# Kernel optimization log

Hardware: AMD Instinct MI355X
Metric: run time of the kernel (lower is better)

Reference implementation:

```python
import jax, jax.numpy as jnp
import numpy as np

SR = 44100
DUR = 2.0
DS = 64
IN_GAIN = 10.0 ** (5.2 / 20.0)


def design_lr4_ir(freq, sr, n_taps=512):
    wc = np.tan(np.pi * freq / sr)
    wc2 = wc * wc
    root2 = np.sqrt(2.0)
    denom = 1 + root2 * wc + wc2
    b_lp = np.array([wc2 / denom, 2 * wc2 / denom, wc2 / denom])
    a_lp = np.array([1.0, 2 * (wc2 - 1) / denom, (1 - root2 * wc + wc2) / denom])
    b_hp = np.array([1 / denom, -2 / denom, 1 / denom])
    a_hp = np.array([1.0, 2 * (wc2 - 1) / denom, (1 - root2 * wc + wc2) / denom])
    b_lp4 = np.convolve(b_lp, b_lp); a_lp4 = np.convolve(a_lp, a_lp)
    b_hp4 = np.convolve(b_hp, b_hp); a_hp4 = np.convolve(a_hp, a_hp)
    def lfilter(b, a, x):
        y = np.zeros_like(x)
        for n in range(len(x)):
            acc = 0.0
            for i in range(len(b)):
                if n - i >= 0:
                    acc += b[i] * x[n - i]
            for i in range(1, len(a)):
                if n - i >= 0:
                    acc -= a[i] * y[n - i]
            y[n] = acc
        return y
    imp = np.zeros(n_taps); imp[0] = 1.0
    return lfilter(b_lp4, a_lp4, imp), lfilter(b_hp4, a_hp4, imp)


def _fir(x, w):
    # x: [B,C,T], w: flipped IR [K]; causal (left) padding, same filter per channel (grouped)
    K = w.shape[0]; C = x.shape[1]
    xp = jnp.pad(x, ((0, 0), (0, 0), (K - 1, 0)))
    kern = jnp.broadcast_to(w.reshape(1, 1, K), (C, 1, K))
    return jax.lax.conv_general_dilated(xp, kern, (1,), 'VALID',
                                        dimension_numbers=('NCH', 'OIH', 'NCH'),
                                        feature_group_count=C)


def _conv1d(x, w, b, pad, dil):
    y = jax.lax.conv_general_dilated(x, w, (1,), [(pad, pad)], rhs_dilation=(dil,),
                                     dimension_numbers=('NCH', 'OIH', 'NCH'))
    return y + b[None, :, None]


def _knee(x, thr, slope, k):
    diff = x - thr
    g_knee = slope * (diff + k / 2) ** 2 / (2 * k)
    return jnp.where(jnp.abs(diff) <= k / 2, g_knee,
                     jnp.where(diff > k / 2, slope * diff, jnp.zeros_like(x)))


def _forward(audio, params, rel_alphas, knee_db, ir_low_lp, ir_low_hp, ir_high_lp, ir_high_hp,
             w0, b0, w1, b1, w2, b2, w3, b3, w4, b4):
    batch, C, T = audio.shape
    audio_in = audio * IN_GAIN
    ott = params[:, -7:]
    amount = ott[:, 0][:, None, None]
    # 3-band LR4 crossover via 512-tap FIRs
    low = _fir(audio_in, ir_low_lp)
    m_h = _fir(audio_in, ir_low_hp)
    mid = _fir(m_h, ir_high_lp)
    high = _fir(m_h, ir_high_hp)
    bands = jnp.stack([high, mid, low], axis=1)            # [B,3,2,T]
    b_flat = bands.reshape(batch * 3, C, T)
    x_sq = jnp.mean(b_flat ** 2, axis=1, keepdims=True)    # [B3,1,T]
    Tc = T // DS
    x_rms = jnp.sqrt(x_sq[..., :Tc * DS].reshape(batch * 3, 1, Tc, DS).mean(-1) + 1e-7)
    # release-only envelope follower via cummax trick (faithful to torch code incl. repeat order)
    rel = jnp.repeat(rel_alphas, batch).reshape(-1, 1, 1)
    k = 1.0 - rel
    idx = jnp.arange(Tc, dtype=x_rms.dtype)
    kp = k ** idx
    ki = k ** (-idx)
    env_c = jax.lax.cummax(x_rms * ki, axis=2) * kp        # [B3,1,Tc]
    # linear interp back to T (align_corners=True)
    pos = jnp.arange(T, dtype=jnp.float32) * ((Tc - 1) / (T - 1))
    i0 = jnp.clip(jnp.floor(pos).astype(jnp.int32), 0, Tc - 2)
    frac = pos - i0.astype(jnp.float32)
    env = jnp.take(env_c, i0, axis=2) * (1 - frac) + jnp.take(env_c, i0 + 1, axis=2) * frac
    env_db = 20.0 * jnp.log10(env + 1e-7).reshape(batch, 3, T)
    t_a = jnp.stack([ott[:, 3], ott[:, 2], ott[:, 1]], axis=1)[..., None]
    t_b = jnp.stack([ott[:, 6], ott[:, 5], ott[:, 4]], axis=1)[..., None]
    above_slopes = jnp.array([1.0, 1.0 - 1 / 66.7, 1.0 - 1 / 66.7], jnp.float32).reshape(1, 3, 1)
    below_slope = jnp.float32(1.0 - 1.0 / 4.17)
    g_db = -_knee(env_db, t_a, above_slopes, knee_db) + _knee(-env_db, -t_b, below_slope, knee_db)
    out_gains = jnp.array([10.3, 5.7, 10.3], jnp.float32).reshape(1, 3, 1)
    total_g = 10.0 ** (jnp.clip(g_db + out_gains, -80.0, 40.0) / 20.0)
    combined = (bands * total_g[:, :, None, :]).sum(axis=1)  # [B,2,T]
    g = lambda z: jax.nn.gelu(z, approximate=False)
    r = g(_conv1d(combined, w0, b0, 1, 1))
    r = g(_conv1d(r, w1, b1, 2, 2))
    r = g(_conv1d(r, w2, b2, 4, 4))
    r = g(_conv1d(r, w3, b3, 8, 8))
    res = _conv1d(r, w4, b4, 1, 1)
    return (1.0 - amount) * audio + amount * (combined + res)


def setup_inputs() -> dict:
    B = 8
    T = int(SR * DUR)
    key = jax.random.key(0)
    ks = jax.random.split(key, 16)
    audio = jax.random.normal(ks[0], (B, 2, T), jnp.float32)
    amount = jax.random.uniform(ks[1], (B, 1), jnp.float32)
    thr = jax.random.uniform(ks[2], (B, 6), jnp.float32, minval=-40.0, maxval=0.0)
    params = jnp.concatenate([amount, thr], axis=1)
    ir_lp1, ir_hp1 = design_lr4_ir(88.3, SR)
    ir_lp2, ir_hp2 = design_lr4_ir(2500.0, SR)
    flip = lambda ir: jnp.asarray(ir[::-1].copy(), jnp.float32)
    sr_c = SR / DS
    rel_alphas = jnp.asarray(1.0 - np.exp(-1.0 / (sr_c * np.array([132.0, 282.0, 282.0]) / 1000.0)), jnp.float32)
    knee_db = jnp.float32(3.0)
    shapes = [(64, 2, 3), (64, 64, 3), (64, 64, 3), (64, 64, 3), (2, 64, 3)]
    out = {
        'audio': audio, 'params': params, 'rel_alphas': rel_alphas, 'knee_db': knee_db,
        'ir_low_lp': flip(ir_lp1), 'ir_low_hp': flip(ir_hp1),
        'ir_high_lp': flip(ir_lp2), 'ir_high_hp': flip(ir_hp2),
    }
    for i, (o, ci, kk) in enumerate(shapes):
        bound = 1.0 / np.sqrt(ci * kk)
        scale = 0.01 if i == len(shapes) - 1 else 1.0
        out[f'w{i}'] = jax.random.uniform(ks[4 + 2 * i], (o, ci, kk), jnp.float32, -bound, bound) * scale
        out[f'b{i}'] = jax.random.uniform(ks[5 + 2 * i], (o,), jnp.float32, -bound, bound) * scale
    return out


def reference(audio, params, rel_alphas, knee_db, ir_low_lp, ir_low_hp, ir_high_lp, ir_high_hp,
              w0, b0, w1, b1, w2, b2, w3, b3, w4, b4):
    return _forward(audio, params, rel_alphas, knee_db, ir_low_lp, ir_low_hp, ir_high_lp, ir_high_hp,
                    w0, b0, w1, b1, w2, b2, w3, b3, w4, b4)
```

## Files before the change

### kernel.cpp

```cpp
#include <hip/hip_runtime.h>
#include <math.h>

#define NT 88200
#define NB 8
#define TC 1378

static constexpr float IN_GAIN_F = 1.8197008586099834f;

#define OFF_A0    3072
#define OFF_A4    4096
#define OFF_ABF   5632
#define OFF_BANDS 24064
#define OFF_XRMS  4257664
#define OFF_ENV   4290736
#define OFF_WHL   4290736

typedef __attribute__((ext_vector_type(8))) short short8v;
typedef __attribute__((ext_vector_type(4))) short short4v;
typedef __attribute__((ext_vector_type(4))) float float4v;
typedef __attribute__((ext_vector_type(16))) float float16v;

__device__ __forceinline__ float gelus(float x) {
  float e = __builtin_amdgcn_exp2f(-2.4554670f * x);
  return x * __builtin_amdgcn_rcpf(1.f + e);
}
__device__ __forceinline__ short f2bf(float x) {
  unsigned int u = __float_as_uint(x);
  u += 0x7fffu + ((u >> 16) & 1u);
  return (short)(u >> 16);
}
__device__ __forceinline__ short f2bft(float x) {
  return (short)(__float_as_uint(x) >> 16);
}
__device__ __forceinline__ float bf2f(short s) {
  return __uint_as_float(((unsigned int)(unsigned short)s) << 16);
}

__global__ __launch_bounds__(256) void k_prep(
    const float* __restrict__ irLL, const float* __restrict__ irLH,
    const float* __restrict__ irHL, const float* __restrict__ irHH,
    const float* __restrict__ w0, const float* __restrict__ w1,
    const float* __restrict__ w2, const float* __restrict__ w3,
    const float* __restrict__ w4, float* __restrict__ ws)
{
  int gid = blockIdx.x * 256 + threadIdx.x;
  int task = blockIdx.y;
  if (task == 0) {
    short* whl = (short*)(ws + OFF_WHL);
    if (gid < 3072) {
      int band = gid >> 10, j = gid & 1023;
      float v = 0.f;
      if (j < 1023) {
        if (band == 2) {
          v = (j >= 511) ? irLL[j - 511] : 0.f;
        } else {
          const float* wb = (band == 0) ? irHH : irHL;
          int lo = j - 511; if (lo < 0) lo = 0;
          int hi = (j < 511) ? j : 511;
          float acc = 0.f;
          for (int i = lo; i <= hi; ++i) acc += irLH[i] * wb[j - i];
          v = acc;
        }
      }
      int entry = band * 1152 + 64 + j;
      short h = f2bf(v);
      whl[entry] = h;
      whl[entry + 4608] = f2bf(v - bf2f(h));
    } else if (gid < 4608) {
      int z = gid - 3072;
      int entry;
      if (z < 384) {
        int band = z >> 7, r = z & 127;
        entry = band * 1152 + (r < 64 ? r : 1024 + r);
      } else {
        entry = 3 * 1152 + (z - 384);
      }
      whl[entry] = 0;
      whl[entry + 4608] = 0;
    }
  } else if (task == 1) {
    if (gid >= 2048) return;
    int wq = gid >> 9;
    int lane = (gid >> 3) & 63;
    int j = gid & 7;
    int l16 = lane & 15, q = lane >> 4;
    int m = wq * 16 + l16;
    int K = q * 8 + j;
    float val = (K < 6) ? w0[(m * 2 + (K & 1)) * 3 + (K >> 1)] : 0.f;
    ((short*)(ws + OFF_A0))[gid] = f2bf(val);
  } else if (task == 2) {
    if (gid >= 3072) return;
    int s = gid >> 9;
    int lane = (gid - s * 512) >> 3;
    int j = gid & 7;
    int m = lane & 15, q = lane >> 4;
    int K = s * 32 + q * 8 + j;
    int k = K >> 6, ic = K & 63;
    float val = (m < 2) ? w4[(m * 64 + ic) * 3 + k] : 0.f;
    ((short*)(ws + OFF_A4))[gid] = f2bf(val);
  } else if (task == 6) {
    for (int r = 0; r < 3; ++r) {
      int i = gid * 3 + r;
      if (i < 24 * TC) ws[OFF_XRMS + i] = 0.f;
    }
  } else {
    int l = task - 3;
    if (gid >= 12288) return;
    const float* wl = (l == 0) ? w1 : (l == 1) ? w2 : w3;
    int ocg = gid / 6144;
    int rem = gid - ocg * 6144;
    int s = rem / 512;
    int rem2 = rem - s * 512;
    int lane = rem2 >> 3;
    int j = gid & 7;
    int m = ocg * 32 + (lane & 31);
    int k = s * 16 + ((lane >> 5) << 3) + j;
    int tap = k >> 6, ic = k & 63;
    short* ap = (short*)(ws + OFF_ABF);
    ap[l * 12288 + gid] = f2bf(wl[(m * 64 + ic) * 3 + tap]);
  }
}

#define FT 320
__global__ __launch_bounds__(256) void k_firm(const float* __restrict__ audio,
                                              float* __restrict__ ws)
{
  __shared__ short xh[4][1360];
  __shared__ __align__(16) short wt[9216];
  __shared__ float ssum[3][5];
  int bc = blockIdx.x, tile = blockIdx.y;
  int t0b = tile * FT;
  int tid = threadIdx.x;
  if (tid < 15) ssum[tid / 5][tid % 5] = 0.f;
  const uint4* wsrc = (const uint4*)((const short*)(ws + OFF_WHL));
  uint4* wdst = (uint4*)wt;
  for (int i = tid; i < 1152; i += 256) wdst[i] = wsrc[i];
  const float* x = audio + bc * NT;
  for (int i = tid; i < 1363; i += 256) {
    int g = t0b - 1022 + i;
    float v = (g >= 0 && g < NT) ? x[g] * IN_GAIN_F : 0.f;
    short h = f2bf(v);
#pragma unroll
    for (int c = 0; c < 4; ++c) {
      int idx = i - c;
      if (idx >= 0 && idx < 1360) xh[c][idx] = h;
    }
  }
  __syncthreads();

  int wave = tid >> 6, lane = tid & 63;
  int q = lane >> 4, l16 = lane & 15;
  int band = (l16 >= 10) ? 2 : (l16 >= 5 ? 1 : 0);
  if (l16 == 15) band = 3;
  int u = l16 - band * 5;
  const short* pAh = wt + band * 1152 + 64 + q * 8 - u * 16;
  const short* pAl = pAh + 4608;
  int c = l16 & 3;
  int xoff = wave * 80 + q * 8 + ((l16 >> 2) << 2);
  const short* pBh = &xh[c][xoff];
  float4v a0 = {0.f, 0.f, 0.f, 0.f};
  float4v a1 = {0.f, 0.f, 0.f, 0.f};
#pragma unroll 2
  for (int s = 0; s < 34; ++s) {
    short8v ah = *(const short8v*)(pAh + 32 * s);
    short8v al = *(const short8v*)(pAl + 32 * s);
    short4v bh0 = *(const short4v*)(pBh + 32 * s);
    short4v bh1 = *(const short4v*)(pBh + 32 * s + 4);
    short8v bh = __builtin_shufflevector(bh0, bh1, 0, 1, 2, 3, 4, 5, 6, 7);
    a0 = __builtin_amdgcn_mfma_f32_16x16x32_bf16(ah, bh, a0, 0, 0, 0);
    a1 = __builtin_amdgcn_mfma_f32_16x16x32_bf16(al, bh, a1, 0, 0, 0);
  }
  float acc[4];
#pragma unroll
  for (int r = 0; r < 4; ++r) acc[r] = a0[r] + a1[r];

  int b = bc >> 1, ch = bc & 1;
  float* bands = ws + OFF_BANDS;
#pragma unroll
  for (int r = 0; r < 4; ++r) {
    int m = q * 4 + r;
    if (m < 15) {
      int bnd = (m >= 10) ? 2 : (m >= 5 ? 1 : 0);
      int uu = m - bnd * 5;
      int t = t0b + wave * 80 + uu * 16 + l16;
      if (t < NT) bands[((b * 3 + bnd) * 2 + ch) * NT + t] = acc[r];
    }
  }

  float s2[4];
#pragma unroll
  for (int r = 0; r < 4; ++r) {
    int m = q * 4 + r;
    s2[r] = (m < 15) ? acc[r] * acc[r] : 0.f;
  }
#pragma unroll
  for (int mask = 1; mask < 16; mask <<= 1)
#pragma unroll
    for (int r = 0; r < 4; ++r)
      s2[r] += __shfl_xor(s2[r], mask, 16);
  if (l16 == 0) {
#pragma unroll
    for (int r = 0; r < 4; ++r) {
      int m = q * 4 + r;
      if (m < 15) {
        int bnd = (m >= 10) ? 2 : (m >= 5 ? 1 : 0);
        int uu = m - bnd * 5;
        int jloc = (wave * 80 + uu * 16) >> 6;
        atomicAdd(&ssum[bnd][jloc], s2[r]);
      }
    }
  }
  __syncthreads();
  if (tid < 15) {
    int bnd = tid / 5, jl = tid - bnd * 5;
    int jg = tile * 5 + jl;
    if (jg < TC) atomicAdd(&ws[OFF_XRMS + (b * 3 + bnd) * TC + jg], ssum[bnd][jl]);
  }
}

__global__ __launch_bounds__(256) void k_scan(const float* __restrict__ rel_alphas,
                                              float* __restrict__ ws)
{
  __shared__ float pA[256], pB[256];
  int row = blockIdx.x;
  int tid = threadIdx.x;
  float kdec = 1.f - rel_alphas[row >> 3];
  const float* xr = ws + OFF_XRMS + row * TC;
  float v[6];
  int base = tid * 6;
#pragma unroll
  for (int s = 0; s < 6; ++s) {
    int j = base + s;
    v[s] = (j < TC) ? sqrtf(xr[j] * (0.5f / 64.f) + 1e-7f) : 0.f;
  }
  float r = v[0];
#pragma unroll
  for (int s = 1; s < 6; ++s) r = fmaxf(v[s], r * kdec);
  pA[tid] = r;
  __syncthreads();
  float k2 = kdec * kdec, k3 = k2 * kdec;
  float kp = k3 * k3;
  float* in = pA; float* outp = pB;
  for (int off = 1; off < 256; off <<= 1) {
    float val = in[tid];
    if (tid >= off) val = fmaxf(val, in[tid - off] * kp);
    outp[tid] = val;
    kp *= kp;
    __syncthreads();
    float* tmp = in; in = outp; outp = tmp;
  }
  float* env = ws + OFF_ENV + row * TC;
  float rr;
  if (tid > 0) {
    float carry = in[tid - 1];
    rr = fmaxf(v[0], carry * kdec);
  } else {
    rr = v[0];
  }
  if (base < TC) env[base] = rr;
#pragma unroll
  for (int s = 1; s < 6; ++s) {
    rr = fmaxf(v[s], rr * kdec);
    if (base + s < TC) env[base + s] = rr;
  }
}

#define PITCH 72
#define SPAN 128
#define TILE 96

__device__ __forceinline__ void mfma_layer32(const short* in, short* outb,
    const short* __restrict__ apk, const float* __restrict__ bias,
    const int d, int t0, int ocg, int posg, int lane)
{
  int l32 = lane & 31, hi = lane >> 5;
  float16v acc;
#pragma unroll
  for (int g = 0; g < 4; ++g) {
    float4 bv = *(const float4*)&bias[ocg * 32 + hi * 4 + g * 8];
    acc[4 * g + 0] = bv.x; acc[4 * g + 1] = bv.y;
    acc[4 * g + 2] = bv.z; acc[4 * g + 3] = bv.w;
  }
  int rbase = posg * 32 + l32;
  int rlo = rbase - d; rlo = rlo < 0 ? 0 : rlo;
  int rhi = rbase + d; rhi = rhi > SPAN - 1 ? SPAN - 1 : rhi;
  const short* pLo  = in + rlo * PITCH + hi * 8;
  const short* pMid = in + rbase * PITCH + hi * 8;
  const short* pHi  = in + rhi * PITCH + hi * 8;
  const short* ap = apk + (ocg * 12 * 64 + lane) * 8;
#pragma unroll
  for (int s = 0; s < 12; ++s) {
    short8v a = *(const short8v*)(ap + s * 512);
    int tap = s >> 2;
    const short* p = (tap == 0) ? pLo : (tap == 1) ? pMid : pHi;
    short8v bf = *(const short8v*)(p + (s & 3) * 16);
    acc = __builtin_amdgcn_mfma_f32_32x32x16_bf16(a, bf, acc, 0, 0, 0);
  }
  int t = t0 - 16 + rbase;
  bool z = (t < 0) | (t >= NT);
  short* wp = outb + rbase * PITCH + ocg * 32 + hi * 4;
#pragma unroll
  for (int g = 0; g < 4; ++g) {
    short4v r;
#pragma unroll
    for (int q = 0; q < 4; ++q)
      r[q] = f2bft(z ? 0.f : gelus(acc[4 * g + q]));
    *(short4v*)(wp + g * 8) = r;
  }
}

__global__ __launch_bounds__(512, 8) void k_convnet(
    const float* __restrict__ audio, const float* __restrict__ params,
    const float* __restrict__ kneep,
    const float* __restrict__ b0, const float* __restrict__ b1,
    const float* __restrict__ b2, const float* __restrict__ b3,
    const float* __restrict__ b4, const float* __restrict__ ws,
    float* __restrict__ out)
{
  __shared__ float cmb[2][SPAN];
  __shared__ __align__(16) char ubuf[SPAN * 8 * 2];
  __shared__ __align__(16) short actA[SPAN * PITCH];
  __shared__ __align__(16) short actB[SPAN * PITCH];
  float* gbuf = (float*)ubuf;
  short (*bfL0)[8] = (short(*)[8])ubuf;
  int tile = blockIdx.x, b = blockIdx.y;
  int t0 = tile * TILE;
  int tid = threadIdx.x;
  int wave = tid >> 6, lane = tid & 63;

  if (tid < 3 * SPAN) {
    int band = tid / SPAN, pos = tid - band * SPAN;
    int t = t0 - 16 + pos;
    float g = 0.f;
    if (t >= 0 && t < NT) {
      const float* env = ws + OFF_ENV;
      float knee = kneep[0];
      float halfk = 0.5f * knee;
      float inv2k = 1.f / (2.f * knee);
      const float scale = (float)(1377.0 / 88199.0);
      float pos_f = (float)t * scale;
      int i0 = (int)floorf(pos_f);
      i0 = i0 < 0 ? 0 : (i0 > TC - 2 ? TC - 2 : i0);
      float frac = pos_f - (float)i0;
      const int tacol[3] = {3, 2, 1};
      const int tbcol[3] = {6, 5, 4};
      const float asl[3] = {1.f, (float)(1.0 - 1.0 / 66.7), (float)(1.0 - 1.0 / 66.7)};
      const float bsl = (float)(1.0 - 1.0 / 4.17);
      const float og[3] = {10.3f, 5.7f, 10.3f};
      int row = b * 3 + band;
      float e = env[row * TC + i0] * (1.f - frac) + env[row * TC + i0 + 1] * frac;
      float edb = 6.0205999132796239f * __builtin_amdgcn_logf(e + 1e-7f);
      float ta = params[b * 7 + tacol[band]];
      float tb = params[b * 7 + tbcol[band]];
      float d1 = edb - ta;
      float gk1 = asl[band] * (d1 + halfk) * (d1 + halfk) * inv2k;
      float ka = (fabsf(d1) <= halfk) ? gk1 : (d1 > halfk ? asl[band] * d1 : 0.f);
      float d2 = tb - edb;
      float gk2 = bsl * (d2 + halfk) * (d2 + halfk) * inv2k;
      float kb = (fabsf(d2) <= halfk) ? gk2 : (d2 > halfk ? bsl * d2 : 0.f);
      float gdb = -ka + kb + og[band];
      gdb = fminf(fmaxf(gdb, -80.f), 40.f);
      g = __builtin_amdgcn_exp2f(gdb * 0.16609640474436812f);
    }
    gbuf[band * SPAN + pos] = g;
  }
  __syncthreads();

  if (tid < SPAN) {
    int t = t0 - 16 + tid;
    float c0 = 0.f, c1 = 0.f;
    if (t >= 0 && t < NT) {
      const float* bands = ws + OFF_BANDS;
#pragma unroll
      for (int band = 0; band < 3; ++band) {
        int row = b * 3 + band;
        float g = gbuf[band * SPAN + tid];
        c0 += bands[(row * 2 + 0) * NT + t] * g;
        c1 += bands[(row * 2 + 1) * NT + t] * g;
      }
    }
    cmb[0][tid] = c0;
    cmb[1][tid] = c1;
  }
  __syncthreads();

  for (int i = tid; i < SPAN * 8; i += 512) {
    int r = i >> 3, j = i & 7;
    short v = 0;
    if (j < 6) {
      int k = j >> 1, ic = j & 1;
      int src = r - 1 + k;
      if (src >= 0 && src < SPAN) v = f2bf(cmb[ic][src]);
    }
    bfL0[r][j] = v;
  }
  __syncthreads();

  int quad = lane >> 4, l16 = lane & 15;

  {
    int wq = wave & 3, half = wave >> 2;
    const short* ap0 = (const short*)(ws + OFF_A0);
    short8v a0 = *(const short8v*)&ap0[(wq * 64 + lane) * 8];
    float4 bv = *(const float4*)&b0[wq * 16 + quad * 4];
    float4v acc[4];
#pragma unroll
    for (int n = 0; n < 4; ++n) { acc[n][0] = bv.x; acc[n][1] = bv.y; acc[n][2] = bv.z; acc[n][3] = bv.w; }
    short8v zf = {0, 0, 0, 0, 0, 0, 0, 0};
#pragma unroll
    for (int n = 0; n < 4; ++n) {
      int row = (half * 4 + n) * 16 + l16;
      short8v bf = (quad == 0) ? *(const short8v*)&bfL0[row][0] : zf;
      acc[n] = __builtin_amdgcn_mfma_f32_16x16x32_bf16(a0, bf, acc[n], 0, 0, 0);
    }
    int ocb = wq * 16 + quad * 4;
#pragma unroll
    for (int n = 0; n < 4; ++n) {
      int p = (half * 4 + n) * 16 + l16;
      int t = t0 - 16 + p;
      bool z = (t < 0) | (t >= NT);
      short4v r;
#pragma unroll
      for (int rg = 0; rg < 4; ++rg)
        r[rg] = f2bft(z ? 0.f : gelus(acc[n][rg]));
      *(short4v*)&actA[p * PITCH + ocb] = r;
    }
  }
  __syncthreads();

  int ocg = wave & 1, posg = wave >> 1;
  const short* apk = (const short*)(ws + OFF_ABF);
  mfma_layer32(actA, actB, apk,          b1, 2, t0, ocg, posg, lane);
  __syncthreads();
  mfma_layer32(actB, actA, apk + 12288,  b2, 4, t0, ocg, posg, lane);
  __syncthreads();
  mfma_layer32(actA, actB, apk + 24576,  b3, 8, t0, ocg, posg, lane);
  __syncthreads();

  if (wave < 6) {
    const short* ap4 = (const short*)(ws + OFF_A4);
    float4v acc = {0.f, 0.f, 0.f, 0.f};
    if (quad == 0) { acc[0] = b4[0]; acc[1] = b4[1]; }
#pragma unroll
    for (int s = 0; s < 6; ++s) {
      short8v a4 = *(const short8v*)&ap4[(s * 64 + lane) * 8];
      int kt = s >> 1;
      int ic0 = (s & 1) * 32 + quad * 8;
      int row = 16 + wave * 16 + l16 + kt - 1;
      short8v bf = *(const short8v*)&actB[row * PITCH + ic0];
      acc = __builtin_amdgcn_mfma_f32_16x16x32_bf16(a4, bf, acc, 0, 0, 0);
    }
    if (quad == 0) {
      int t = t0 + wave * 16 + l16;
      if (t < NT) {
        float amt = params[b * 7];
#pragma unroll
        for (int r = 0; r < 2; ++r) {
          float aud = audio[(b * 2 + r) * NT + t];
          out[(b * 2 + r) * NT + t] =
              (1.f - amt) * aud + amt * (cmb[r][16 + wave * 16 + l16] + acc[r]);
        }
      }
    }
  }
}

extern "C" void kernel_launch(void* const* d_in, const int* in_sizes, int n_in,
                              void* d_out, int out_size, void* d_ws, size_t ws_size,
                              hipStream_t stream)
{
  (void)in_sizes; (void)n_in; (void)out_size; (void)ws_size;
  const float* audio = (const float*)d_in[0];
  const float* params = (const float*)d_in[1];
  const float* rel   = (const float*)d_in[2];
  const float* knee  = (const float*)d_in[3];
  const float* irLL  = (const float*)d_in[4];
  const float* irLH  = (const float*)d_in[5];
  const float* irHL  = (const float*)d_in[6];
  const float* irHH  = (const float*)d_in[7];
  const float* w0 = (const float*)d_in[8];  const float* b0 = (const float*)d_in[9];
  const float* w1 = (const float*)d_in[10]; const float* b1 = (const float*)d_in[11];
  const float* w2 = (const float*)d_in[12]; const float* b2 = (const float*)d_in[13];
  const float* w3 = (const float*)d_in[14]; const float* b3 = (const float*)d_in[15];
  const float* w4 = (const float*)d_in[16]; const float* b4 = (const float*)d_in[17];
  float* out = (float*)d_out;
  float* ws  = (float*)d_ws;

  hipLaunchKernelGGL(k_prep, dim3(48, 7), dim3(256), 0, stream,
                     irLL, irLH, irHL, irHH, w0, w1, w2, w3, w4, ws);
  hipLaunchKernelGGL(k_firm, dim3(16, 276), dim3(256), 0, stream, audio, ws);
  hipLaunchKernelGGL(k_scan, dim3(24), dim3(256), 0, stream, rel, ws);
  hipLaunchKernelGGL(k_convnet, dim3(919, 8), dim3(512), 0, stream,
                     audio, params, knee, b0, b1, b2, b3, b4, ws, out);
}
```

Measured before the change: 295.5 us.

## Enlarge convnet tile to 256 positions and pack bf16 conversions

Result: slower. 301.6 us (+2.1%).

```diff
diff --git a/kernel.cpp b/kernel.cpp
--- a/kernel.cpp
+++ b/kernel.cpp
@@ -17,6 +17,7 @@
 
 typedef __attribute__((ext_vector_type(8))) short short8v;
 typedef __attribute__((ext_vector_type(4))) short short4v;
+typedef __attribute__((ext_vector_type(2))) unsigned int uint2v;
 typedef __attribute__((ext_vector_type(4))) float float4v;
 typedef __attribute__((ext_vector_type(16))) float float16v;
 
@@ -29,11 +30,13 @@
   u += 0x7fffu + ((u >> 16) & 1u);
   return (short)(u >> 16);
 }
-__device__ __forceinline__ short f2bft(float x) {
-  return (short)(__float_as_uint(x) >> 16);
-}
 __device__ __forceinline__ float bf2f(short s) {
   return __uint_as_float(((unsigned int)(unsigned short)s) << 16);
+}
+__device__ __forceinline__ unsigned int cvt_pk_bf16(float lo, float hi) {
+  unsigned int d;
+  asm("v_cvt_pk_bf16_f32 %0, %1, %2" : "=v"(d) : "v"(lo), "v"(hi));
+  return d;
 }
 
 __global__ __launch_bounds__(256) void k_prep(
@@ -266,8 +269,8 @@
 }
 
 #define PITCH 72
-#define SPAN 128
-#define TILE 96
+#define SPAN 256
+#define TILE 224
 
 __device__ __forceinline__ void mfma_layer32(const short* in, short* outb,
     const short* __restrict__ apk, const float* __restrict__ bias,
@@ -301,15 +304,18 @@
   short* wp = outb + rbase * PITCH + ocg * 32 + hi * 4;
 #pragma unroll
   for (int g = 0; g < 4; ++g) {
-    short4v r;
-#pragma unroll
-    for (int q = 0; q < 4; ++q)
-      r[q] = f2bft(z ? 0.f : gelus(acc[4 * g + q]));
-    *(short4v*)(wp + g * 8) = r;
-  }
-}
-
-__global__ __launch_bounds__(512, 8) void k_convnet(
+    float v0 = z ? 0.f : gelus(acc[4 * g + 0]);
+    float v1 = z ? 0.f : gelus(acc[4 * g + 1]);
+    float v2 = z ? 0.f : gelus(acc[4 * g + 2]);
+    float v3 = z ? 0.f : gelus(acc[4 * g + 3]);
+    uint2v r;
+    r[0] = cvt_pk_bf16(v0, v1);
+    r[1] = cvt_pk_bf16(v2, v3);
+    *(uint2v*)(wp + g * 8) = r;
+  }
+}
+
+__global__ __launch_bounds__(1024, 8) void k_convnet(
     const float* __restrict__ audio, const float* __restrict__ params,
     const float* __restrict__ kneep,
     const float* __restrict__ b0, const float* __restrict__ b1,
@@ -384,7 +390,7 @@
   }
   __syncthreads();
 
-  for (int i = tid; i < SPAN * 8; i += 512) {
+  for (int i = tid; i < SPAN * 8; i += 1024) {
     int r = i >> 3, j = i & 7;
     short v = 0;
     if (j < 6) {
@@ -419,11 +425,14 @@
       int p = (half * 4 + n) * 16 + l16;
       int t = t0 - 16 + p;
       bool z = (t < 0) | (t >= NT);
-      short4v r;
-#pragma unroll
-      for (int rg = 0; rg < 4; ++rg)
-        r[rg] = f2bft(z ? 0.f : gelus(acc[n][rg]));
-      *(short4v*)&actA[p * PITCH + ocb] = r;
+      float v0 = z ? 0.f : gelus(acc[n][0]);
+      float v1 = z ? 0.f : gelus(acc[n][1]);
+      float v2 = z ? 0.f : gelus(acc[n][2]);
+      float v3 = z ? 0.f : gelus(acc[n][3]);
+      uint2v r;
+      r[0] = cvt_pk_bf16(v0, v1);
+      r[1] = cvt_pk_bf16(v2, v3);
+      *(uint2v*)&actA[p * PITCH + ocb] = r;
     }
   }
   __syncthreads();
@@ -437,7 +446,7 @@
   mfma_layer32(actA, actB, apk + 24576,  b3, 8, t0, ocg, posg, lane);
   __syncthreads();
 
-  if (wave < 6) {
+  if (wave < 14) {
     const short* ap4 = (const short*)(ws + OFF_A4);
     float4v acc = {0.f, 0.f, 0.f, 0.f};
     if (quad == 0) { acc[0] = b4[0]; acc[1] = b4[1]; }
@@ -490,6 +499,6 @@
                      irLL, irLH, irHL, irHH, w0, w1, w2, w3, w4, ws);
   hipLaunchKernelGGL(k_firm, dim3(16, 276), dim3(256), 0, stream, audio, ws);
   hipLaunchKernelGGL(k_scan, dim3(24), dim3(256), 0, stream, rel, ws);
-  hipLaunchKernelGGL(k_convnet, dim3(919, 8), dim3(512), 0, stream,
+  hipLaunchKernelGGL(k_convnet, dim3(394, 8), dim3(1024), 0, stream,
                      audio, params, knee, b0, b1, b2, b3, b4, ws, out);
 }
```
